# Kernel optimization log

Measured on AMD Instinct MI355X. Metric: run time of the kernel, lower is better.

## Reference

```python
import jax, jax.numpy as jnp
import numpy as np

N, E, F_IN, H, C = 50000, 800000, 128, 128, 64


def setup_inputs() -> dict:
    key = jax.random.key(0)
    ks = jax.random.split(key, 10)
    s = lambda f: np.float32(1.0 / np.sqrt(f))
    return {
        "x": jax.random.normal(ks[0], (N, F_IN), jnp.float32),
        "edge_index": jax.random.randint(ks[1], (2, E), 0, N, dtype=jnp.int64),
        # SAGEConv1: lin_l (on aggregated neighbors, with bias) + lin_r (on root, no bias)
        "W1l": jax.random.normal(ks[2], (F_IN, H), jnp.float32) * s(F_IN),
        "b1l": jnp.zeros((H,), jnp.float32),
        "W1r": jax.random.normal(ks[3], (F_IN, H), jnp.float32) * s(F_IN),
        # SAGEConv2
        "W2l": jax.random.normal(ks[4], (H, C), jnp.float32) * s(H),
        "b2l": jnp.zeros((C,), jnp.float32),
        "W2r": jax.random.normal(ks[5], (H, C), jnp.float32) * s(H),
        # GCNConv
        "Wg": jax.random.normal(ks[6], (C, C), jnp.float32) * s(C),
        "bg": jnp.zeros((C,), jnp.float32),
    }


def sage_conv(x, edge_index, Wl, bl, Wr):
    # PyG SAGEConv (mean aggr): out = lin_l(mean_{j in N(i)} x_j) + lin_r(x_i)
    n = x.shape[0]
    src, dst = edge_index[0], edge_index[1]
    agg = jax.ops.segment_sum(x[src], dst, num_segments=n)  # [N, F]
    cnt = jax.ops.segment_sum(jnp.ones((src.shape[0],), x.dtype), dst, num_segments=n)
    mean = agg / jnp.maximum(cnt, 1.0)[:, None]
    return mean @ Wl + bl + x @ Wr


def gcn_conv(x, edge_index, W, b):
    # PyG GCNConv: add self loops, symmetric normalization D^-1/2 A D^-1/2
    n = x.shape[0]
    loop = jnp.arange(n, dtype=edge_index.dtype)
    src = jnp.concatenate([edge_index[0], loop])
    dst = jnp.concatenate([edge_index[1], loop])
    deg = jax.ops.segment_sum(jnp.ones((src.shape[0],), x.dtype), dst, num_segments=n)
    dinv = jnp.where(deg > 0, jax.lax.rsqrt(jnp.maximum(deg, 1e-12)), 0.0)
    norm = dinv[src] * dinv[dst]  # [E+N]
    xw = x @ W
    out = jax.ops.segment_sum(xw[src] * norm[:, None], dst, num_segments=n)
    return out + b


def reference(x, edge_index, W1l, b1l, W1r, W2l, b2l, W2r, Wg, bg):
    h = jax.nn.relu(sage_conv(x, edge_index, W1l, b1l, W1r))
    # dropout is identity in eval mode
    h = sage_conv(h, edge_index, W2l, b2l, W2r)
    h = jax.nn.softmax(h, axis=1)  # activate='softmax'
    return gcn_conv(h, edge_index, Wg, bg)
```

## Files before the change

### kernel.cpp

```cpp
#include <hip/hip_runtime.h>
#include <hip/hip_fp16.h>
#include <math.h>


typedef __attribute__((ext_vector_type(8))) short bf16x8;
typedef __attribute__((ext_vector_type(4))) float f32x4;
typedef __attribute__((ext_vector_type(2))) float f32v2;

__device__ inline unsigned short f32_bf16_hi(float f) {
    unsigned int u = __builtin_bit_cast(unsigned int, f);
    u = (u + 0x7FFFu + ((u >> 16) & 1u)) >> 16;
    return (unsigned short)u;
}
__device__ inline float bf16_to_f32(unsigned short h) {
    unsigned int u = ((unsigned int)h) << 16;
    return __builtin_bit_cast(float, u);
}

union H8 { float4 f4; __half2 h[4]; };

__global__ void count_kernel(const int* __restrict__ dst, int* __restrict__ off,
                             int E, int NB, int BK) {
    __shared__ int hist[256];
    int t = threadIdx.x;
    hist[t] = 0;
    __syncthreads();
    int base = blockIdx.x * 8192;
    for (int i = t; i < 8192; i += 256) {
        int e = base + i;
        if (e < E) atomicAdd(&hist[dst[e] >> 8], 1);
    }
    __syncthreads();
    if (t < BK) off[1 + t * NB + blockIdx.x] = hist[t];
    if (blockIdx.x == 0 && t == 0) off[0] = 0;
}

__global__ void scan_reduce_kernel(const int* __restrict__ data, int* __restrict__ bsum, int n) {
    __shared__ int red[256];
    int t = threadIdx.x;
    int base = blockIdx.x * 2048 + t * 8;
    int s = 0;
    if (base + 8 <= n) {
        int4 a = *(const int4*)(data + base);
        int4 b = *(const int4*)(data + base + 4);
        s = a.x + a.y + a.z + a.w + b.x + b.y + b.z + b.w;
    } else {
        for (int i = 0; i < 8; ++i)
            if (base + i < n) s += data[base + i];
    }
    red[t] = s;
    __syncthreads();
    for (int off = 128; off > 0; off >>= 1) {
        if (t < off) red[t] += red[t + off];
        __syncthreads();
    }
    if (t == 0) bsum[blockIdx.x] = red[0];
}

__global__ void scan_offsets_kernel(int* __restrict__ bsum, int B) {
    if (threadIdx.x == 0 && blockIdx.x == 0) {
        int run = 0;
        for (int i = 0; i < B; ++i) { int v = bsum[i]; bsum[i] = run; run += v; }
    }
}

__global__ void scan_final_kernel(int* __restrict__ data, const int* __restrict__ bsum, int n) {
    __shared__ int tsum[256];
    int t = threadIdx.x;
    int base = blockIdx.x * 2048 + t * 8;
    int v[8];
    int s = 0;
#pragma unroll
    for (int i = 0; i < 8; ++i) {
        v[i] = (base + i < n) ? data[base + i] : 0;
        s += v[i];
    }
    tsum[t] = s;
    for (int off = 1; off < 256; off <<= 1) {
        __syncthreads();
        int u = (t >= off) ? tsum[t - off] : 0;
        __syncthreads();
        tsum[t] += u;
    }
    __syncthreads();
    int run = bsum[blockIdx.x] + tsum[t] - s;
#pragma unroll
    for (int i = 0; i < 8; ++i) {
        run += v[i];
        if (base + i < n) data[base + i] = run;
    }
}

__global__ void partition_kernel(const int* __restrict__ src, const int* __restrict__ dst,
                                 const int* __restrict__ off, unsigned* __restrict__ ebuf,
                                 int E, int NB, int BK) {
    __shared__ int cur[256];
    int t = threadIdx.x;
    if (t < BK) cur[t] = off[t * NB + blockIdx.x];
    __syncthreads();
    int base = blockIdx.x * 8192;
    for (int i = t; i < 8192; i += 256) {
        int e = base + i;
        if (e < E) {
            int d = dst[e];
            int pos = atomicAdd(&cur[d >> 8], 1);
            ebuf[pos] = ((unsigned)src[e] << 8) | (unsigned)(d & 255);
        }
    }
}

__global__ void finalize_kernel(const unsigned* __restrict__ ebuf, const int* __restrict__ off,
                                int* __restrict__ col, int* __restrict__ rowptr,
                                float* __restrict__ dinv, int N, int NB, int E) {
    __shared__ int hist[256], scn[256], cur[256];
    int b = blockIdx.x, t = threadIdx.x;
    int base = off[b * NB];
    int end  = off[(b + 1) * NB];
    int M = end - base;
    hist[t] = 0;
    __syncthreads();
    for (int i = t; i < M; i += 256) atomicAdd(&hist[ebuf[base + i] & 255u], 1);
    __syncthreads();
    scn[t] = hist[t];
    for (int o = 1; o < 256; o <<= 1) {
        __syncthreads();
        int u = (t >= o) ? scn[t - o] : 0;
        __syncthreads();
        scn[t] += u;
    }
    __syncthreads();
    int excl = scn[t] - hist[t];
    int node = b * 256 + t;
    if (node < N) {
        rowptr[node] = base + excl;
        dinv[node] = rsqrtf((float)(hist[t] + 1));
    }
    if (b == 0 && t == 0) rowptr[N] = E;
    cur[t] = base + excl;
    __syncthreads();
    for (int i = t; i < M; i += 256) {
        unsigned w = ebuf[base + i];
        int pos = atomicAdd(&cur[w & 255u], 1);
        col[pos] = (int)(w >> 8);
    }
}

__global__ void packw_kernel(const float* __restrict__ W1l, const float* __restrict__ W1r,
                             const float* __restrict__ W2l, const float* __restrict__ W2r,
                             const float* __restrict__ Wg,
                             unsigned short* __restrict__ p1h, unsigned short* __restrict__ p1l,
                             unsigned short* __restrict__ p2h, unsigned short* __restrict__ p2l,
                             unsigned short* __restrict__ p3h, unsigned short* __restrict__ p3l) {
    int which = blockIdx.y;
    const float* W;
    unsigned short *hi, *lo;
    int K, Mp, colOff, T;
    if (which == 0)      { W = W1l; hi = p1h; lo = p1l; K = 128; Mp = 128; colOff = 0;   T = 16; }
    else if (which == 1) { W = W1r; hi = p1h; lo = p1l; K = 128; Mp = 128; colOff = 128; T = 16; }
    else if (which == 2) { W = W2l; hi = p2h; lo = p2l; K = 128; Mp = 64;  colOff = 0;   T = 8;  }
    else if (which == 3) { W = W2r; hi = p2h; lo = p2l; K = 128; Mp = 64;  colOff = 64;  T = 8;  }
    else                 { W = Wg;  hi = p3h; lo = p3l; K = 64;  Mp = 64;  colOff = 0;   T = 4;  }
    int idx = blockIdx.x * blockDim.x + threadIdx.x;
    if (idx >= K * Mp) return;
    int k = idx / Mp, m = idx % Mp;
    float w = W[(size_t)k * Mp + m];
    int colI = colOff + m;
    int s = k >> 5, kk = k & 31, qq = kk >> 3, j = kk & 7;
    int tt = colI >> 4, n = colI & 15;
    int lane = qq * 16 + n;
    size_t pos = ((size_t)(s * T + tt) * 64 + lane) * 8 + j;
    unsigned short h = f32_bf16_hi(w);
    hi[pos] = h;
    lo[pos] = f32_bf16_hi(w - bf16_to_f32(h));
}

__launch_bounds__(256)
__global__ void gemm1_kernel(const float* __restrict__ A,
                             const unsigned short* __restrict__ Whi,
                             const unsigned short* __restrict__ Wlo,
                             unsigned char* __restrict__ outA8, __half* __restrict__ outB, int N) {
    constexpr int Ttot = 16, TB = 8;
    __shared__ __align__(16) unsigned char pk[4][16][128];
    const int lane = threadIdx.x & 63;
    const int wave = threadIdx.x >> 6;
    const int m = lane & 15, q = lane >> 4;
    const int t0 = blockIdx.y * TB;
    const int row0 = blockIdx.x * 64 + wave * 16;
    int arow = row0 + m;
    if (arow >= N) arow = N - 1;
    const float* ap = A + (size_t)arow * 128 + q * 8;

    float av[4][8];
#pragma unroll
    for (int s = 0; s < 4; ++s) {
        *(float4*)(av[s])     = *(const float4*)(ap + s * 32);
        *(float4*)(av[s] + 4) = *(const float4*)(ap + s * 32 + 4);
    }
    bf16x8 ahi[4], alo[4];
#pragma unroll
    for (int s = 0; s < 4; ++s)
#pragma unroll
        for (int i = 0; i < 8; ++i) {
            unsigned short h = f32_bf16_hi(av[s][i]);
            ahi[s][i] = (short)h;
            alo[s][i] = (short)f32_bf16_hi(av[s][i] - bf16_to_f32(h));
        }

    f32x4 acc[TB];
#pragma unroll
    for (int t = 0; t < TB; ++t) acc[t] = (f32x4)(0.f);
    const bf16x8* whp = (const bf16x8*)Whi;
    const bf16x8* wlp = (const bf16x8*)Wlo;
#pragma unroll
    for (int s = 0; s < 4; ++s) {
        const int base = (s * Ttot + t0) * 64 + lane;
#pragma unroll
        for (int t = 0; t < TB; ++t) {
            bf16x8 wh = whp[base + t * 64];
            bf16x8 wl = wlp[base + t * 64];
            acc[t] = __builtin_amdgcn_mfma_f32_16x16x32_bf16(ahi[s], wh, acc[t], 0, 0, 0);
            acc[t] = __builtin_amdgcn_mfma_f32_16x16x32_bf16(alo[s], wh, acc[t], 0, 0, 0);
            acc[t] = __builtin_amdgcn_mfma_f32_16x16x32_bf16(ahi[s], wl, acc[t], 0, 0, 0);
        }
    }

    if (blockIdx.y == 0) {
#pragma unroll
        for (int r = 0; r < 4; ++r) {
            int row = q * 4 + r;
            int sw = (row & 3) << 5;
#pragma unroll
            for (int t = 0; t < 8; t += 2) {
                int w = __builtin_amdgcn_cvt_pk_fp8_f32(acc[t][r], acc[t + 1][r], 0, false);
                pk[wave][row][(t * 16 + m) ^ sw] = (unsigned char)(w & 0xff);
                pk[wave][row][((t + 1) * 16 + m) ^ sw] = (unsigned char)((w >> 8) & 0xff);
            }
        }
        __syncthreads();
        int rr = lane >> 2, qt = lane & 3;
        int grow = row0 + rr;
        if (grow < N) {
            const unsigned char* srcp = &pk[wave][rr][(qt ^ (rr & 3)) * 32];
            uint4 v0 = *(const uint4*)(srcp);
            uint4 v1 = *(const uint4*)(srcp + 16);
            *(uint4*)(outA8 + (size_t)grow * 128 + qt * 32) = v0;
            *(uint4*)(outA8 + (size_t)grow * 128 + qt * 32 + 16) = v1;
        }
    } else {
#pragma unroll
        for (int r = 0; r < 4; ++r) {
            int row = row0 + q * 4 + r;
            if (row < N) {
#pragma unroll
                for (int t = 0; t < TB; ++t) {
                    int c = (t0 + t) * 16 + m - 128;
                    outB[(size_t)row * 128 + c] = __float2half(acc[t][r]);
                }
            }
        }
    }
}

__launch_bounds__(256)
__global__ void sage2_fused_kernel(const unsigned char* __restrict__ p8, const __half* __restrict__ q16,
                                   const int* __restrict__ rowptr, const int* __restrict__ col,
                                   const float* __restrict__ b1l,
                                   const unsigned short* __restrict__ Whi,
                                   const unsigned short* __restrict__ Wlo,
                                   __half* __restrict__ r16, __half* __restrict__ s16, int N) {
    __shared__ float part[4][64][16];
    const int lane = threadIdx.x & 63;
    const int wave = threadIdx.x >> 6;
    const int pairH = wave & 1;
    const int grp   = wave >> 1;
    const int m = lane & 15, q = lane >> 4;
    const int row0 = blockIdx.x * 32 + grp * 16;
    int node = row0 + m;
    int nclamp = (node < N) ? node : (N - 1);
    int sAll = rowptr[nclamp];
    int eAll = (node < N) ? rowptr[nclamp + 1] : sAll;
    int deg  = eAll - sAll;
    int half0 = (deg + 1) >> 1;
    int sIdx = sAll + (pairH ? half0 : 0);
    int eIdx = pairH ? eAll : (sAll + half0);

    float acc[4][8];
#pragma unroll
    for (int s = 0; s < 4; ++s)
#pragma unroll
        for (int i = 0; i < 8; ++i) acc[s][i] = 0.f;

    const unsigned char* pb = p8 + q * 8;
    int ptr = sIdx;
    for (; ptr + 4 <= eIdx; ptr += 4) {
        int j0 = col[ptr], j1 = col[ptr + 1], j2 = col[ptr + 2], j3 = col[ptr + 3];
        uint2 u[4][4];
#pragma unroll
        for (int s = 0; s < 4; ++s) {
            u[0][s] = *(const uint2*)(pb + (size_t)j0 * 128 + s * 32);
            u[1][s] = *(const uint2*)(pb + (size_t)j1 * 128 + s * 32);
            u[2][s] = *(const uint2*)(pb + (size_t)j2 * 128 + s * 32);
            u[3][s] = *(const uint2*)(pb + (size_t)j3 * 128 + s * 32);
        }
#pragma unroll
        for (int s = 0; s < 4; ++s)
#pragma unroll
            for (int e = 0; e < 4; ++e) {
                f32v2 a = __builtin_amdgcn_cvt_pk_f32_fp8(u[e][s].x, false);
                f32v2 b = __builtin_amdgcn_cvt_pk_f32_fp8(u[e][s].x, true);
                f32v2 c = __builtin_amdgcn_cvt_pk_f32_fp8(u[e][s].y, false);
                f32v2 d = __builtin_amdgcn_cvt_pk_f32_fp8(u[e][s].y, true);
                acc[s][0] += a[0]; acc[s][1] += a[1];
                acc[s][2] += b[0]; acc[s][3] += b[1];
                acc[s][4] += c[0]; acc[s][5] += c[1];
                acc[s][6] += d[0]; acc[s][7] += d[1];
            }
    }
    for (; ptr < eIdx; ++ptr) {
        int j0 = col[ptr];
#pragma unroll
        for (int s = 0; s < 4; ++s) {
            uint2 u0 = *(const uint2*)(pb + (size_t)j0 * 128 + s * 32);
            f32v2 a = __builtin_amdgcn_cvt_pk_f32_fp8(u0.x, false);
            f32v2 b = __builtin_amdgcn_cvt_pk_f32_fp8(u0.x, true);
            f32v2 c = __builtin_amdgcn_cvt_pk_f32_fp8(u0.y, false);
            f32v2 d = __builtin_amdgcn_cvt_pk_f32_fp8(u0.y, true);
            acc[s][0] += a[0]; acc[s][1] += a[1];
            acc[s][2] += b[0]; acc[s][3] += b[1];
            acc[s][4] += c[0]; acc[s][5] += c[1];
            acc[s][6] += d[0]; acc[s][7] += d[1];
        }
    }

    float* ap = &acc[0][0];
    const int swz = lane & 3;
#pragma unroll
    for (int c = 0; c < 2; ++c) {
        if (c) __syncthreads();
#pragma unroll
        for (int sl = 0; sl < 4; ++sl)
            *(float4*)&part[wave][lane][(sl ^ swz) * 4] =
                *(const float4*)(ap + (c * 4 + sl) * 4);
        __syncthreads();
#pragma unroll
        for (int sl = 0; sl < 4; ++sl) {
            float4 pv = *(const float4*)&part[wave ^ 1][lane][(sl ^ swz) * 4];
            int g = (c * 4 + sl) * 4;
            ap[g]     += pv.x;
            ap[g + 1] += pv.y;
            ap[g + 2] += pv.z;
            ap[g + 3] += pv.w;
        }
    }

    float inv = 1.0f / fmaxf((float)deg, 1.0f);
    bf16x8 ahi[4], alo[4];
#pragma unroll
    for (int s = 0; s < 4; ++s) {
        H8 qv;
        qv.f4 = *(const float4*)(q16 + (size_t)nclamp * 128 + s * 32 + q * 8);
        float bv[8];
        *(float4*)(bv)     = *(const float4*)(b1l + s * 32 + q * 8);
        *(float4*)(bv + 4) = *(const float4*)(b1l + s * 32 + q * 8 + 4);
#pragma unroll
        for (int i = 0; i < 8; ++i) {
            float qf = __half2float(((const __half*)&qv)[i]);
            float h = fmaxf(acc[s][i] * inv + qf + bv[i], 0.f);
            unsigned short hb = f32_bf16_hi(h);
            ahi[s][i] = (short)hb;
            alo[s][i] = (short)f32_bf16_hi(h - bf16_to_f32(hb));
        }
    }

    f32x4 accm[4];
#pragma unroll
    for (int t = 0; t < 4; ++t) accm[t] = (f32x4)(0.f);
    const bf16x8* whp = (const bf16x8*)Whi;
    const bf16x8* wlp = (const bf16x8*)Wlo;
#pragma unroll
    for (int s = 0; s < 4; ++s) {
        const int base = (s * 8 + pairH * 4) * 64 + lane;
#pragma unroll
        for (int t = 0; t < 4; ++t) {
            bf16x8 wh = whp[base + t * 64];
            bf16x8 wl = wlp[base + t * 64];
            accm[t] = __builtin_amdgcn_mfma_f32_16x16x32_bf16(ahi[s], wh, accm[t], 0, 0, 0);
            accm[t] = __builtin_amdgcn_mfma_f32_16x16x32_bf16(alo[s], wh, accm[t], 0, 0, 0);
            accm[t] = __builtin_amdgcn_mfma_f32_16x16x32_bf16(ahi[s], wl, accm[t], 0, 0, 0);
        }
    }
    __half* op = pairH ? s16 : r16;
#pragma unroll
    for (int r = 0; r < 4; ++r) {
        int row = row0 + q * 4 + r;
        if (row < N) {
#pragma unroll
            for (int t = 0; t < 4; ++t) {
                int c = t * 16 + m;
                op[(size_t)row * 64 + c] = __float2half(accm[t][r]);
            }
        }
    }
}

__launch_bounds__(256)
__global__ void gcn_prep_fused_kernel(const __half* __restrict__ r16, const __half* __restrict__ s16,
                                      const int* __restrict__ rowptr, const int* __restrict__ col,
                                      const float* __restrict__ b2l,
                                      const unsigned short* __restrict__ Whi,
                                      const unsigned short* __restrict__ Wlo,
                                      const float* __restrict__ dinv,
                                      __half* __restrict__ tp16, int N) {
    __shared__ float part[4][64][16];
    const int lane = threadIdx.x & 63;
    const int wave = threadIdx.x >> 6;
    const int pairH = wave & 1;
    const int grp   = wave >> 1;
    const int m = lane & 15, q = lane >> 4;
    const int row0 = blockIdx.x * 32 + grp * 16;
    int node = row0 + m;
    int nclamp = (node < N) ? node : (N - 1);
    int sAll = rowptr[nclamp];
    int eAll = (node < N) ? rowptr[nclamp + 1] : sAll;
    int deg  = eAll - sAll;
    int half0 = (deg + 1) >> 1;
    int sIdx = sAll + (pairH ? half0 : 0);
    int eIdx = pairH ? eAll : (sAll + half0);

    float acc[2][8];
#pragma unroll
    for (int s = 0; s < 2; ++s)
#pragma unroll
        for (int i = 0; i < 8; ++i) acc[s][i] = 0.f;

    const __half* rb = r16 + q * 8;
    int ptr = sIdx;
    for (; ptr + 4 <= eIdx; ptr += 4) {
        int j0 = col[ptr], j1 = col[ptr + 1], j2 = col[ptr + 2], j3 = col[ptr + 3];
        H8 u[4][2];
#pragma unroll
        for (int s = 0; s < 2; ++s) {
            u[0][s].f4 = *(const float4*)(rb + (size_t)j0 * 64 + s * 32);
            u[1][s].f4 = *(const float4*)(rb + (size_t)j1 * 64 + s * 32);
            u[2][s].f4 = *(const float4*)(rb + (size_t)j2 * 64 + s * 32);
            u[3][s].f4 = *(const float4*)(rb + (size_t)j3 * 64 + s * 32);
        }
#pragma unroll
        for (int s = 0; s < 2; ++s)
#pragma unroll
            for (int k = 0; k < 4; ++k) {
                float2 f0 = __half22float2(u[0][s].h[k]);
                float2 f1 = __half22float2(u[1][s].h[k]);
                float2 f2 = __half22float2(u[2][s].h[k]);
                float2 f3 = __half22float2(u[3][s].h[k]);
                acc[s][2 * k]     += (f0.x + f1.x) + (f2.x + f3.x);
                acc[s][2 * k + 1] += (f0.y + f1.y) + (f2.y + f3.y);
            }
    }
    for (; ptr < eIdx; ++ptr) {
        int j0 = col[ptr];
#pragma unroll
        for (int s = 0; s < 2; ++s) {
            H8 u0;
            u0.f4 = *(const float4*)(rb + (size_t)j0 * 64 + s * 32);
#pragma unroll
            for (int k = 0; k < 4; ++k) {
                float2 f0 = __half22float2(u0.h[k]);
                acc[s][2 * k]     += f0.x;
                acc[s][2 * k + 1] += f0.y;
            }
        }
    }

    float* ap = &acc[0][0];
    const int swz = lane & 3;
#pragma unroll
    for (int sl = 0; sl < 4; ++sl)
        *(float4*)&part[wave][lane][(sl ^ swz) * 4] = *(const float4*)(ap + sl * 4);
    __syncthreads();
#pragma unroll
    for (int sl = 0; sl < 4; ++sl) {
        float4 pv = *(const float4*)&part[wave ^ 1][lane][(sl ^ swz) * 4];
        ap[sl * 4]     += pv.x;
        ap[sl * 4 + 1] += pv.y;
        ap[sl * 4 + 2] += pv.z;
        ap[sl * 4 + 3] += pv.w;
    }

    float inv = 1.0f / fmaxf((float)deg, 1.0f);
    float v[2][8];
    float mx = -1e30f;
#pragma unroll
    for (int s = 0; s < 2; ++s) {
        H8 sv;
        sv.f4 = *(const float4*)(s16 + (size_t)nclamp * 64 + s * 32 + q * 8);
        float bv[8];
        *(float4*)(bv)     = *(const float4*)(b2l + s * 32 + q * 8);
        *(float4*)(bv + 4) = *(const float4*)(b2l + s * 32 + q * 8 + 4);
#pragma unroll
        for (int i = 0; i < 8; ++i) {
            float sf = __half2float(((const __half*)&sv)[i]);
            v[s][i] = acc[s][i] * inv + sf + bv[i];
            mx = fmaxf(mx, v[s][i]);
        }
    }
    mx = fmaxf(mx, __shfl_xor(mx, 16, 64));
    mx = fmaxf(mx, __shfl_xor(mx, 32, 64));
    float sm = 0.f;
#pragma unroll
    for (int s = 0; s < 2; ++s)
#pragma unroll
        for (int i = 0; i < 8; ++i) {
            v[s][i] = expf(v[s][i] - mx);
            sm += v[s][i];
        }
    sm += __shfl_xor(sm, 16, 64);
    sm += __shfl_xor(sm, 32, 64);
    float is = 1.0f / sm;

    bf16x8 ahi[2], alo[2];
#pragma unroll
    for (int s = 0; s < 2; ++s)
#pragma unroll
        for (int i = 0; i < 8; ++i) {
            float h = v[s][i] * is;
            unsigned short hb = f32_bf16_hi(h);
            ahi[s][i] = (short)hb;
            alo[s][i] = (short)f32_bf16_hi(h - bf16_to_f32(hb));
        }

    f32x4 accm[2];
#pragma unroll
    for (int t = 0; t < 2; ++t) accm[t] = (f32x4)(0.f);
    const bf16x8* whp = (const bf16x8*)Whi;
    const bf16x8* wlp = (const bf16x8*)Wlo;
#pragma unroll
    for (int s = 0; s < 2; ++s) {
        const int base = (s * 4 + pairH * 2) * 64 + lane;
#pragma unroll
        for (int t = 0; t < 2; ++t) {
            bf16x8 wh = whp[base + t * 64];
            bf16x8 wl = wlp[base + t * 64];
            accm[t] = __builtin_amdgcn_mfma_f32_16x16x32_bf16(ahi[s], wh, accm[t], 0, 0, 0);
            accm[t] = __builtin_amdgcn_mfma_f32_16x16x32_bf16(alo[s], wh, accm[t], 0, 0, 0);
            accm[t] = __builtin_amdgcn_mfma_f32_16x16x32_bf16(ahi[s], wl, accm[t], 0, 0, 0);
        }
    }
#pragma unroll
    for (int r = 0; r < 4; ++r) {
        int row = row0 + q * 4 + r;
        if (row < N) {
            float sc = dinv[row];
#pragma unroll
            for (int t = 0; t < 2; ++t) {
                int c = (pairH * 2 + t) * 16 + m;
                tp16[(size_t)row * 64 + c] = __float2half(accm[t][r] * sc);
            }
        }
    }
}

__global__ void gcn_agg_kernel(const __half* __restrict__ tp,
                               const int* __restrict__ rowptr, const int* __restrict__ col,
                               const float* __restrict__ dinv, const float* __restrict__ bg,
                               float* __restrict__ out, int N) {
    int node = blockIdx.x * 4 + (threadIdx.x >> 6);
    if (node >= N) return;
    int lane = threadIdx.x & 63;
    int f2 = lane & 31;
    int ep = lane >> 5;
    int s = rowptr[node], e = rowptr[node + 1];
    float ax[8], ay[8];
#pragma unroll
    for (int k = 0; k < 8; ++k) { ax[k] = 0.f; ay[k] = 0.f; }
    int p = s;
    for (; p + 16 <= e; p += 16) {
#pragma unroll
        for (int k = 0; k < 8; ++k) {
            int j = col[p + 2 * k + ep];
            float2 f = __half22float2(*(const __half2*)(tp + (size_t)j * 64 + 2 * f2));
            ax[k] += f.x;
            ay[k] += f.y;
        }
    }
    for (int t = p + ep; t < e; t += 2) {
        int j = col[t];
        float2 f = __half22float2(*(const __half2*)(tp + (size_t)j * 64 + 2 * f2));
        ax[0] += f.x;
        ay[0] += f.y;
    }
    float sx = ((ax[0] + ax[1]) + (ax[2] + ax[3])) + ((ax[4] + ax[5]) + (ax[6] + ax[7]));
    float sy = ((ay[0] + ay[1]) + (ay[2] + ay[3])) + ((ay[4] + ay[5]) + (ay[6] + ay[7]));
    sx += __shfl_xor(sx, 32, 64);
    sy += __shfl_xor(sy, 32, 64);
    if (ep == 0) {
        float2 selfv = __half22float2(*(const __half2*)(tp + (size_t)node * 64 + 2 * f2));
        float di = dinv[node];
        float2 o;
        o.x = (sx + selfv.x) * di + bg[2 * f2];
        o.y = (sy + selfv.y) * di + bg[2 * f2 + 1];
        *(float2*)(out + (size_t)node * 64 + 2 * f2) = o;
    }
}

extern "C" void kernel_launch(void* const* d_in, const int* in_sizes, int n_in,
                              void* d_out, int out_size, void* d_ws, size_t ws_size,
                              hipStream_t stream) {
    const float* x = (const float*)d_in[0];
    const int* ei = (const int*)d_in[1];
    const float* W1l = (const float*)d_in[2];
    const float* b1l = (const float*)d_in[3];
    const float* W1r = (const float*)d_in[4];
    const float* W2l = (const float*)d_in[5];
    const float* b2l = (const float*)d_in[6];
    const float* W2r = (const float*)d_in[7];
    const float* Wg  = (const float*)d_in[8];
    const float* bg  = (const float*)d_in[9];

    const int N = in_sizes[0] / 128;
    const int E = in_sizes[1] / 2;
    const int* srcp = ei;
    const int* dstp = ei + E;

    const int NB = (E + 8191) / 8192;
    const int BK = (N + 255) >> 8;
    const int len = BK * NB;

    float* ws = (float*)d_ws;
    float* dinv = ws;
    unsigned char* p8 = (unsigned char*)(dinv + N);
    __half* q16 = (__half*)(p8 + (size_t)N * 128);
    __half* r16 = q16 + (size_t)N * 128;
    __half* s16 = r16 + (size_t)N * 64;
    __half* tp16 = s16 + (size_t)N * 64;
    int* rowptr = (int*)(tp16 + (size_t)N * 64);
    int* off    = rowptr + (N + 1);
    int* colbuf = off + len + 2;
    unsigned* ebuf = (unsigned*)(colbuf + E);
    int* bsum   = (int*)(ebuf + E);
    uintptr_t up = (uintptr_t)(bsum + 32);
    up = (up + 15) & ~(uintptr_t)15;
    unsigned short* p1h = (unsigned short*)up;
    unsigned short* p1l = p1h + 32768;
    unsigned short* p2h = p1l + 32768;
    unsigned short* p2l = p2h + 16384;
    unsigned short* p3h = p2l + 16384;
    unsigned short* p3l = p3h + 4096;

    float* out = (float*)d_out;

    count_kernel<<<NB, 256, 0, stream>>>(dstp, off, E, NB, BK);
    const int sn = len + 1;
    const int SBs = (sn + 2047) / 2048;
    scan_reduce_kernel<<<SBs, 256, 0, stream>>>(off, bsum, sn);
    scan_offsets_kernel<<<1, 64, 0, stream>>>(bsum, SBs);
    scan_final_kernel<<<SBs, 256, 0, stream>>>(off, bsum, sn);
    partition_kernel<<<NB, 256, 0, stream>>>(srcp, dstp, off, ebuf, E, NB, BK);
    finalize_kernel<<<BK, 256, 0, stream>>>(ebuf, off, colbuf, rowptr, dinv, N, NB, E);

    packw_kernel<<<dim3(64, 5), 256, 0, stream>>>(W1l, W1r, W2l, W2r, Wg,
                                                  p1h, p1l, p2h, p2l, p3h, p3l);

    const int gb  = (N + 63) / 64;
    const int gbf = (N + 31) / 32;
    const int ab  = (N + 3) / 4;

    gemm1_kernel<<<dim3(gb, 2), 256, 0, stream>>>(x, p1h, p1l, p8, q16, N);

    sage2_fused_kernel<<<gbf, 256, 0, stream>>>(p8, q16, rowptr, colbuf, b1l,
                                                p2h, p2l, r16, s16, N);

    gcn_prep_fused_kernel<<<gbf, 256, 0, stream>>>(r16, s16, rowptr, colbuf, b2l,
                                                   p3h, p3l, dinv, tp16, N);

    gcn_agg_kernel<<<ab, 256, 0, stream>>>(tp16, rowptr, colbuf, dinv, bg, out, N);
}
```

Measured before the change: 269.7 us.

## Split neighbor gathers across four waves per 16-node tile with permuted fp8 layout

The fused SAGE2 and GCN-prep kernels now give each 16-node tile to a whole block of four waves. Each wave aggregates a quarter of every node's edges, and the partial sums are reduced through shared memory. Each wave then computes a quarter of the output columns with MFMA. The fp8 feature store in gemm1 is permuted so each lane can fetch its 32 contiguous bytes with two 16-byte loads instead of four 8-byte loads. The intent is more wave-level parallelism and wider memory transactions on the irregular gather. The cost is extra cross-wave reduction traffic and twice as many blocks.

Result: slower. 277.3 us (+2.8%).

```diff
diff --git a/kernel.cpp b/kernel.cpp
--- a/kernel.cpp
+++ b/kernel.cpp
@@ -18,6 +18,21 @@
 }
 
 union H8 { float4 f4; __half2 h[4]; };
+
+__device__ inline void dec16(uint4 u, float* a0, float* a1) {
+    f32v2 x0 = __builtin_amdgcn_cvt_pk_f32_fp8(u.x, false);
+    f32v2 x1 = __builtin_amdgcn_cvt_pk_f32_fp8(u.x, true);
+    f32v2 y0 = __builtin_amdgcn_cvt_pk_f32_fp8(u.y, false);
+    f32v2 y1 = __builtin_amdgcn_cvt_pk_f32_fp8(u.y, true);
+    a0[0] += x0[0]; a0[1] += x0[1]; a0[2] += x1[0]; a0[3] += x1[1];
+    a0[4] += y0[0]; a0[5] += y0[1]; a0[6] += y1[0]; a0[7] += y1[1];
+    f32v2 z0 = __builtin_amdgcn_cvt_pk_f32_fp8(u.z, false);
+    f32v2 z1 = __builtin_amdgcn_cvt_pk_f32_fp8(u.z, true);
+    f32v2 w0 = __builtin_amdgcn_cvt_pk_f32_fp8(u.w, false);
+    f32v2 w1 = __builtin_amdgcn_cvt_pk_f32_fp8(u.w, true);
+    a1[0] += z0[0]; a1[1] += z0[1]; a1[2] += z1[0]; a1[3] += z1[1];
+    a1[4] += w0[0]; a1[5] += w0[1]; a1[6] += w1[0]; a1[7] += w1[1];
+}
 
 __global__ void count_kernel(const int* __restrict__ dst, int* __restrict__ off,
                              int E, int NB, int BK) {
@@ -232,8 +247,11 @@
 #pragma unroll
             for (int t = 0; t < 8; t += 2) {
                 int w = __builtin_amdgcn_cvt_pk_fp8_f32(acc[t][r], acc[t + 1][r], 0, false);
-                pk[wave][row][(t * 16 + m) ^ sw] = (unsigned char)(w & 0xff);
-                pk[wave][row][((t + 1) * 16 + m) ^ sw] = (unsigned char)((w >> 8) & 0xff);
+                int off = (t >> 1) * 8 + (m & 7);
+                int c0 = ((2 * t + (m >> 3)) & 3) * 32 + off;
+                int c1 = ((2 * t + 2 + (m >> 3)) & 3) * 32 + off;
+                pk[wave][row][c0 ^ sw] = (unsigned char)(w & 0xff);
+                pk[wave][row][c1 ^ sw] = (unsigned char)((w >> 8) & 0xff);
             }
         }
         __syncthreads();
@@ -270,19 +288,16 @@
                                    __half* __restrict__ r16, __half* __restrict__ s16, int N) {
     __shared__ float part[4][64][16];
     const int lane = threadIdx.x & 63;
-    const int wave = threadIdx.x >> 6;
-    const int pairH = wave & 1;
-    const int grp   = wave >> 1;
+    const int w = threadIdx.x >> 6;
     const int m = lane & 15, q = lane >> 4;
-    const int row0 = blockIdx.x * 32 + grp * 16;
+    const int row0 = blockIdx.x * 16;
     int node = row0 + m;
     int nclamp = (node < N) ? node : (N - 1);
     int sAll = rowptr[nclamp];
     int eAll = (node < N) ? rowptr[nclamp + 1] : sAll;
     int deg  = eAll - sAll;
-    int half0 = (deg + 1) >> 1;
-    int sIdx = sAll + (pairH ? half0 : 0);
-    int eIdx = pairH ? eAll : (sAll + half0);
+    int sIdx = sAll + ((deg * w) >> 2);
+    int eIdx = sAll + ((deg * (w + 1)) >> 2);
 
     float acc[4][8];
 #pragma unroll
@@ -290,46 +305,31 @@
 #pragma unroll
         for (int i = 0; i < 8; ++i) acc[s][i] = 0.f;
 
-    const unsigned char* pb = p8 + q * 8;
+    const unsigned char* pb = p8 + q * 32;
     int ptr = sIdx;
     for (; ptr + 4 <= eIdx; ptr += 4) {
         int j0 = col[ptr], j1 = col[ptr + 1], j2 = col[ptr + 2], j3 = col[ptr + 3];
-        uint2 u[4][4];
-#pragma unroll
-        for (int s = 0; s < 4; ++s) {
-            u[0][s] = *(const uint2*)(pb + (size_t)j0 * 128 + s * 32);
-            u[1][s] = *(const uint2*)(pb + (size_t)j1 * 128 + s * 32);
-            u[2][s] = *(const uint2*)(pb + (size_t)j2 * 128 + s * 32);
-            u[3][s] = *(const uint2*)(pb + (size_t)j3 * 128 + s * 32);
-        }
-#pragma unroll
-        for (int s = 0; s < 4; ++s)
-#pragma unroll
-            for (int e = 0; e < 4; ++e) {
-                f32v2 a = __builtin_amdgcn_cvt_pk_f32_fp8(u[e][s].x, false);
-                f32v2 b = __builtin_amdgcn_cvt_pk_f32_fp8(u[e][s].x, true);
-                f32v2 c = __builtin_amdgcn_cvt_pk_f32_fp8(u[e][s].y, false);
-                f32v2 d = __builtin_amdgcn_cvt_pk_f32_fp8(u[e][s].y, true);
-                acc[s][0] += a[0]; acc[s][1] += a[1];
-                acc[s][2] += b[0]; acc[s][3] += b[1];
-                acc[s][4] += c[0]; acc[s][5] += c[1];
-                acc[s][6] += d[0]; acc[s][7] += d[1];
-            }
+        uint4 uA[4], uB[4];
+        uA[0] = *(const uint4*)(pb + (size_t)j0 * 128);
+        uB[0] = *(const uint4*)(pb + (size_t)j0 * 128 + 16);
+        uA[1] = *(const uint4*)(pb + (size_t)j1 * 128);
+        uB[1] = *(const uint4*)(pb + (size_t)j1 * 128 + 16);
+        uA[2] = *(const uint4*)(pb + (size_t)j2 * 128);
+        uB[2] = *(const uint4*)(pb + (size_t)j2 * 128 + 16);
+        uA[3] = *(const uint4*)(pb + (size_t)j3 * 128);
+        uB[3] = *(const uint4*)(pb + (size_t)j3 * 128 + 16);
+#pragma unroll
+        for (int e = 0; e < 4; ++e) {
+            dec16(uA[e], acc[0], acc[1]);
+            dec16(uB[e], acc[2], acc[3]);
+        }
     }
     for (; ptr < eIdx; ++ptr) {
         int j0 = col[ptr];
-#pragma unroll
-        for (int s = 0; s < 4; ++s) {
-            uint2 u0 = *(const uint2*)(pb + (size_t)j0 * 128 + s * 32);
-            f32v2 a = __builtin_amdgcn_cvt_pk_f32_fp8(u0.x, false);
-            f32v2 b = __builtin_amdgcn_cvt_pk_f32_fp8(u0.x, true);
-            f32v2 c = __builtin_amdgcn_cvt_pk_f32_fp8(u0.y, false);
-            f32v2 d = __builtin_amdgcn_cvt_pk_f32_fp8(u0.y, true);
-            acc[s][0] += a[0]; acc[s][1] += a[1];
-            acc[s][2] += b[0]; acc[s][3] += b[1];
-            acc[s][4] += c[0]; acc[s][5] += c[1];
-            acc[s][6] += d[0]; acc[s][7] += d[1];
-        }
+        uint4 uA = *(const uint4*)(pb + (size_t)j0 * 128);
+        uint4 uB = *(const uint4*)(pb + (size_t)j0 * 128 + 16);
+        dec16(uA, acc[0], acc[1]);
+        dec16(uB, acc[2], acc[3]);
     }
 
     float* ap = &acc[0][0];
@@ -339,17 +339,20 @@
         if (c) __syncthreads();
 #pragma unroll
         for (int sl = 0; sl < 4; ++sl)
-            *(float4*)&part[wave][lane][(sl ^ swz) * 4] =
+            *(float4*)&part[w][lane][(sl ^ swz) * 4] =
                 *(const float4*)(ap + (c * 4 + sl) * 4);
         __syncthreads();
 #pragma unroll
-        for (int sl = 0; sl < 4; ++sl) {
-            float4 pv = *(const float4*)&part[wave ^ 1][lane][(sl ^ swz) * 4];
-            int g = (c * 4 + sl) * 4;
-            ap[g]     += pv.x;
-            ap[g + 1] += pv.y;
-            ap[g + 2] += pv.z;
-            ap[g + 3] += pv.w;
+        for (int p = 1; p < 4; ++p) {
+#pragma unroll
+            for (int sl = 0; sl < 4; ++sl) {
+                float4 pv = *(const float4*)&part[w ^ p][lane][(sl ^ swz) * 4];
+                int g = (c * 4 + sl) * 4;
+                ap[g]     += pv.x;
+                ap[g + 1] += pv.y;
+                ap[g + 2] += pv.z;
+                ap[g + 3] += pv.w;
+            }
         }
     }
 
@@ -372,16 +375,16 @@
         }
     }
 
-    f32x4 accm[4];
-#pragma unroll
-    for (int t = 0; t < 4; ++t) accm[t] = (f32x4)(0.f);
+    f32x4 accm[2];
+#pragma unroll
+    for (int t = 0; t < 2; ++t) accm[t] = (f32x4)(0.f);
     const bf16x8* whp = (const bf16x8*)Whi;
     const bf16x8* wlp = (const bf16x8*)Wlo;
 #pragma unroll
     for (int s = 0; s < 4; ++s) {
-        const int base = (s * 8 + pairH * 4) * 64 + lane;
-#pragma unroll
-        for (int t = 0; t < 4; ++t) {
+        const int base = (s * 8 + 2 * w) * 64 + lane;
+#pragma unroll
+        for (int t = 0; t < 2; ++t) {
             bf16x8 wh = whp[base + t * 64];
             bf16x8 wl = wlp[base + t * 64];
             accm[t] = __builtin_amdgcn_mfma_f32_16x16x32_bf16(ahi[s], wh, accm[t], 0, 0, 0);
@@ -389,14 +392,14 @@
             accm[t] = __builtin_amdgcn_mfma_f32_16x16x32_bf16(ahi[s], wl, accm[t], 0, 0, 0);
         }
     }
-    __half* op = pairH ? s16 : r16;
+    __half* op = (w >= 2) ? s16 : r16;
 #pragma unroll
     for (int r = 0; r < 4; ++r) {
         int row = row0 + q * 4 + r;
         if (row < N) {
 #pragma unroll
-            for (int t = 0; t < 4; ++t) {
-                int c = t * 16 + m;
+            for (int t = 0; t < 2; ++t) {
+                int c = ((2 * w + t) * 16 + m) & 63;
                 op[(size_t)row * 64 + c] = __float2half(accm[t][r]);
             }
         }
@@ -413,19 +416,16 @@
                                       __half* __restrict__ tp16, int N) {
     __shared__ float part[4][64][16];
     const int lane = threadIdx.x & 63;
-    const int wave = threadIdx.x >> 6;
-    const int pairH = wave & 1;
-    const int grp   = wave >> 1;
+    const int w = threadIdx.x >> 6;
     const int m = lane & 15, q = lane >> 4;
-    const int row0 = blockIdx.x * 32 + grp * 16;
+    const int row0 = blockIdx.x * 16;
     int node = row0 + m;
     int nclamp = (node < N) ? node : (N - 1);
     int sAll = rowptr[nclamp];
     int eAll = (node < N) ? rowptr[nclamp + 1] : sAll;
     int deg  = eAll - sAll;
-    int half0 = (deg + 1) >> 1;
-    int sIdx = sAll + (pairH ? half0 : 0);
-    int eIdx = pairH ? eAll : (sAll + half0);
+    int sIdx = sAll + ((deg * w) >> 2);
+    int eIdx = sAll + ((deg * (w + 1)) >> 2);
 
     float acc[2][8];
 #pragma unroll
@@ -476,15 +476,18 @@
     const int swz = lane & 3;
 #pragma unroll
     for (int sl = 0; sl < 4; ++sl)
-        *(float4*)&part[wave][lane][(sl ^ swz) * 4] = *(const float4*)(ap + sl * 4);
-    __syncthreads();
-#pragma unroll
-    for (int sl = 0; sl < 4; ++sl) {
-        float4 pv = *(const float4*)&part[wave ^ 1][lane][(sl ^ swz) * 4];
-        ap[sl * 4]     += pv.x;
-        ap[sl * 4 + 1] += pv.y;
-        ap[sl * 4 + 2] += pv.z;
-        ap[sl * 4 + 3] += pv.w;
+        *(float4*)&part[w][lane][(sl ^ swz) * 4] = *(const float4*)(ap + sl * 4);
+    __syncthreads();
+#pragma unroll
+    for (int p = 1; p < 4; ++p) {
+#pragma unroll
+        for (int sl = 0; sl < 4; ++sl) {
+            float4 pv = *(const float4*)&part[w ^ p][lane][(sl ^ swz) * 4];
+            ap[sl * 4]     += pv.x;
+            ap[sl * 4 + 1] += pv.y;
+            ap[sl * 4 + 2] += pv.z;
+            ap[sl * 4 + 3] += pv.w;
+        }
     }
 
     float inv = 1.0f / fmaxf((float)deg, 1.0f);
@@ -529,33 +532,25 @@
             alo[s][i] = (short)f32_bf16_hi(h - bf16_to_f32(hb));
         }
 
-    f32x4 accm[2];
-#pragma unroll
-    for (int t = 0; t < 2; ++t) accm[t] = (f32x4)(0.f);
+    f32x4 accm = (f32x4)(0.f);
     const bf16x8* whp = (const bf16x8*)Whi;
     const bf16x8* wlp = (const bf16x8*)Wlo;
 #pragma unroll
     for (int s = 0; s < 2; ++s) {
-        const int base = (s * 4 + pairH * 2) * 64 + lane;
-#pragma unroll
-        for (int t = 0; t < 2; ++t) {
-            bf16x8 wh = whp[base + t * 64];
-            bf16x8 wl = wlp[base + t * 64];
-            accm[t] = __builtin_amdgcn_mfma_f32_16x16x32_bf16(ahi[s], wh, accm[t], 0, 0, 0);
-            accm[t] = __builtin_amdgcn_mfma_f32_16x16x32_bf16(alo[s], wh, accm[t], 0, 0, 0);
-            accm[t] = __builtin_amdgcn_mfma_f32_16x16x32_bf16(ahi[s], wl, accm[t], 0, 0, 0);
-        }
+        const int base = (s * 4 + w) * 64 + lane;
+        bf16x8 wh = whp[base];
+        bf16x8 wl = wlp[base];
+        accm = __builtin_amdgcn_mfma_f32_16x16x32_bf16(ahi[s], wh, accm, 0, 0, 0);
+        accm = __builtin_amdgcn_mfma_f32_16x16x32_bf16(alo[s], wh, accm, 0, 0, 0);
+        accm = __builtin_amdgcn_mfma_f32_16x16x32_bf16(ahi[s], wl, accm, 0, 0, 0);
     }
 #pragma unroll
     for (int r = 0; r < 4; ++r) {
         int row = row0 + q * 4 + r;
         if (row < N) {
             float sc = dinv[row];
-#pragma unroll
-            for (int t = 0; t < 2; ++t) {
-                int c = (pairH * 2 + t) * 16 + m;
-                tp16[(size_t)row * 64 + c] = __float2half(accm[t][r] * sc);
-            }
+            int c = w * 16 + m;
+            tp16[(size_t)row * 64 + c] = __float2half(accm[r] * sc);
         }
     }
 }
@@ -662,7 +657,7 @@
                                                   p1h, p1l, p2h, p2l, p3h, p3l);
 
     const int gb  = (N + 63) / 64;
-    const int gbf = (N + 31) / 32;
+    const int gbf = (N + 15) / 16;
     const int ab  = (N + 3) / 4;
 
     gemm1_kernel<<<dim3(gb, 2), 256, 0, stream>>>(x, p1h, p1l, p8, q16, N);
```
